# Performance work log

Measured on AMD Instinct MI355X. Metric: run time of the kernel, lower is better.

## Reference

```python
import jax, jax.numpy as jnp
import numpy as np

B, T, D, H = 4, 2048, 1024, 16
HD = D // H  # head_dim = 64


def setup_inputs() -> dict:
    key = jax.random.key(0)
    k1, k2, k3 = jax.random.split(key, 3)
    x = jax.random.normal(k1, (B, T, D), dtype=jnp.float32)
    # torch Linear weights: [out_features, in_features], kaiming-ish scale
    Wqkv = jax.random.normal(k2, (3 * D, D), dtype=jnp.float32) * (1.0 / np.sqrt(D))
    Wout = jax.random.normal(k3, (D, D), dtype=jnp.float32) * (1.0 / np.sqrt(D))
    return {"x": x, "Wqkv": Wqkv, "Wout": Wout}


def reference(x, Wqkv, Wout):
    b, t, c = x.shape
    qkv = x @ Wqkv.T                      # [B,T,3D]
    q, k, v = jnp.split(qkv, 3, axis=2)
    # [B,T,D] -> [B,H,T,HD]
    q = q.reshape(b, t, H, HD).transpose(0, 2, 1, 3)
    k = k.reshape(b, t, H, HD).transpose(0, 2, 1, 3)
    v = v.reshape(b, t, H, HD).transpose(0, 2, 1, 3)
    scale = 1.0 / np.sqrt(HD).astype(np.float32)
    att = jnp.einsum('bhqd,bhkd->bhqk', q, k) * scale  # [B,H,T,T]
    causal = jnp.tril(jnp.ones((t, t), dtype=bool))
    att = jnp.where(causal[None, None], att, -jnp.inf)
    att = jax.nn.softmax(att, axis=-1)
    y = jnp.einsum('bhqk,bhkd->bhqd', att, v)          # [B,H,T,HD]
    y = y.transpose(0, 2, 1, 3).reshape(b, t, c)       # [B,T,D]
    return y @ Wout.T
```

## Files before the change

### kernel.cpp

```cpp
#include <hip/hip_runtime.h>
#include <hip/hip_bf16.h>
#include <stdint.h>

#define B_ 4
#define T_ 2048
#define D_ 1024
#define H_ 16
#define M_ (B_*T_)
#define N1_ (3*D_)

typedef __attribute__((ext_vector_type(8))) short short8;
typedef __attribute__((ext_vector_type(4))) short short4v;
typedef __attribute__((ext_vector_type(4))) float f32x4;
typedef __attribute__((ext_vector_type(16))) float f32x16;

typedef const __attribute__((address_space(1))) void* as1cp;
typedef __attribute__((address_space(3))) void* as3p;

__device__ __forceinline__ ushort f2bf(float f) {
  union { float f; unsigned u; } v; v.f = f;
  unsigned r = v.u + 0x7fffu + ((v.u >> 16) & 1u);
  return (ushort)(r >> 16);
}

__global__ void cast_f32_bf16(const float* __restrict__ in, ushort* __restrict__ out, int n4) {
  int i = blockIdx.x * blockDim.x + threadIdx.x;
  int stride = gridDim.x * blockDim.x;
  for (; i < n4; i += stride) {
    float4 v = reinterpret_cast<const float4*>(in)[i];
    ushort4 o;
    o.x = f2bf(v.x); o.y = f2bf(v.y); o.z = f2bf(v.z); o.w = f2bf(v.w);
    reinterpret_cast<ushort4*>(out)[i] = o;
  }
}

__device__ __forceinline__ void gload_lds16(const ushort* g, ushort* l) {
  __builtin_amdgcn_global_load_lds((as1cp)(const void*)g, (as3p)(void*)l, 16, 0, 0);
}

__device__ __forceinline__ short4v ds_tr16(unsigned addr) {
  short4v r;
  asm volatile("ds_read_b64_tr_b16 %0, %1" : "=v"(r) : "v"(addr) : "memory");
  return r;
}

__device__ __forceinline__ short8 cat8(short4v a, short4v b) {
  short8 r;
  r[0]=a[0]; r[1]=a[1]; r[2]=a[2]; r[3]=a[3];
  r[4]=b[0]; r[5]=b[1]; r[6]=b[2]; r[7]=b[3];
  return r;
}

__device__ __forceinline__ unsigned cvtpk(float lo, float hi) {
  unsigned r;
  asm("v_cvt_pk_bf16_f32 %0, %1, %2" : "=v"(r) : "v"(lo), "v"(hi));
  return r;
}

__device__ __forceinline__ f32x16 mfma32(short8 a, short8 b, f32x16 c) {
  return __builtin_amdgcn_mfma_f32_32x32x16_bf16(a, b, c, 0, 0, 0);
}

template<int MODE>
__global__ __launch_bounds__(256) void gemm_bt(const ushort* __restrict__ A,
                                               const ushort* __restrict__ Bm,
                                               void* __restrict__ Cout,
                                               int M, int N, int K) {
  __shared__ ushort Al[128*32];
  __shared__ ushort Bl[128*32];
  const int tid  = threadIdx.x;
  const int lane = tid & 63;
  const int w    = tid >> 6;
  const int g    = lane >> 4;
  const int ln   = lane & 15;
  const int m0 = blockIdx.y * 128;
  const int n0 = blockIdx.x * 128;
  const int wr = w >> 1, wc = w & 1;

  f32x4 acc[4][4] = {};

  for (int kt = 0; kt < K; kt += 32) {
    __syncthreads();
    #pragma unroll
    for (int j = 0; j < 2; ++j) {
      int cc  = w * 2 + j;
      int idx = cc * 64 + lane;
      int row = idx >> 2;
      int kofs = (idx & 3) * 8;
      gload_lds16(A  + (size_t)(m0 + row) * K + kt + kofs, &Al[cc * 512]);
      gload_lds16(Bm + (size_t)(n0 + row) * K + kt + kofs, &Bl[cc * 512]);
    }
    __syncthreads();
    short8 a[4], b[4];
    #pragma unroll
    for (int m = 0; m < 4; ++m)
      a[m] = *(const short8*)&Al[(wr*64 + m*16 + ln) * 32 + g*8];
    #pragma unroll
    for (int n = 0; n < 4; ++n)
      b[n] = *(const short8*)&Bl[(wc*64 + n*16 + ln) * 32 + g*8];
    #pragma unroll
    for (int m = 0; m < 4; ++m)
      #pragma unroll
      for (int n = 0; n < 4; ++n)
        acc[m][n] = __builtin_amdgcn_mfma_f32_16x16x32_bf16(a[m], b[n], acc[m][n], 0, 0, 0);
  }

  #pragma unroll
  for (int m = 0; m < 4; ++m) {
    int gr = m0 + wr*64 + m*16 + g*4;
    #pragma unroll
    for (int n = 0; n < 4; ++n) {
      int gc = n0 + wc*64 + n*16 + ln;
      #pragma unroll
      for (int r = 0; r < 4; ++r) {
        float v = acc[m][n][r];
        if (MODE == 2 && gc < 1024) v *= 0.18033688011112042f;
        if (MODE) ((ushort*)Cout)[(size_t)(gr + r) * N + gc] = f2bf(v);
        else      ((float*)Cout)[(size_t)(gr + r) * N + gc]  = v;
      }
    }
  }
}

__global__ __launch_bounds__(512, 2) void attn7(const ushort* __restrict__ qkv,
                                                ushort* __restrict__ y) {
  __shared__ ushort Kl[2][4096];
  __shared__ ushort Vl[2][4096];

  const int tid  = threadIdx.x;
  const int lane = tid & 63;
  const int w    = tid >> 6;
  const int l31  = lane & 31;
  const int hi   = lane >> 5;

  const int bh = blockIdx.x;
  const int b  = bh >> 4;
  const int h  = bh & 15;
  const int qb = 7 - (int)blockIdx.y;
  const int rowg = b * T_;
  const int q0 = qb * 256;
  const int qw = q0 + w * 32;
  const int qrow = qw + l31;
  const int nt = 4 * qb + 4;

  const int krow  = tid >> 3;
  const int kslot = tid & 7;
  const int kcb   = (kslot * 16) ^ ((krow & 7) << 4);
  const int vdh = tid & 1, vr = (tid >> 1) & 3, vg = (tid >> 3) & 3,
            vkq = (tid >> 5) & 1, vks = (tid >> 6) & 3, vdt = (tid >> 8) & 1;
  const int vkey = vks*16 + vkq*8 + (vg >> 1)*4 + vr;
  const int vdd  = vdt*32 + (vg & 1)*16 + vdh*8;

  short8 qf[4];
  {
    const ushort* qp = qkv + (size_t)(rowg + qrow) * N1_ + h*64 + hi*8;
    #pragma unroll
    for (int kc = 0; kc < 4; ++kc) qf[kc] = *(const short8*)(qp + kc*16);
  }

  f32x16 oacc[2] = {};
  float lrun = 0.f;

  const unsigned VbBase = (unsigned)(size_t)(as3p)(void*)&Vl[0][0];
  const unsigned trln = (unsigned)(((lane >> 4) * 128) + (lane & 15) * 8);

  gload_lds16(qkv + (size_t)(rowg + 0 + krow) * N1_ + D_ + h*64 + (kcb >> 1), &Kl[0][w*512]);
  gload_lds16(qkv + (size_t)(rowg + 0 + vkey) * N1_ + 2*D_ + h*64 + vdd,      &Vl[0][w*512]);

  for (int kt = 0; kt < nt; ++kt) {
    const int buf = kt & 1;
    const int kbase = kt * 64;
    if (kt + 1 < nt) {
      const int kb2 = kbase + 64;
      gload_lds16(qkv + (size_t)(rowg + kb2 + krow) * N1_ + D_ + h*64 + (kcb >> 1), &Kl[buf^1][w*512]);
      gload_lds16(qkv + (size_t)(rowg + kb2 + vkey) * N1_ + 2*D_ + h*64 + vdd,      &Vl[buf^1][w*512]);
      asm volatile("s_waitcnt vmcnt(2)" ::: "memory");
    } else {
      asm volatile("s_waitcnt vmcnt(0)" ::: "memory");
    }
    asm volatile("s_barrier" ::: "memory");

    const bool act = (kbase <= qw + 31);
    if (act) {
      f32x16 sv[2] = {};
      const char* Kb = (const char*)&Kl[buf][0];
      __builtin_amdgcn_s_setprio(1);
      #pragma unroll
      for (int kc = 0; kc < 4; ++kc) {
        unsigned co = (unsigned)((kc*32 + hi*16) ^ ((l31 & 7) << 4));
        short8 k0 = *(const short8*)(Kb + (size_t)l31*128 + co);
        short8 k1 = *(const short8*)(Kb + (size_t)(32 + l31)*128 + co);
        sv[0] = mfma32(k0, qf[kc], sv[0]);
        sv[1] = mfma32(k1, qf[kc], sv[1]);
      }
      __builtin_amdgcn_s_setprio(0);

      if (kbase + 63 > qw) {
        #pragma unroll
        for (int t = 0; t < 2; ++t)
          #pragma unroll
          for (int r = 0; r < 16; ++r) {
            int kl = kbase + t*32 + (r & 3) + 8*(r >> 2) + 4*hi;
            if (kl > qrow) sv[t][r] = -1.0e38f;
          }
      }

      #pragma unroll
      for (int t = 0; t < 2; ++t)
        #pragma unroll
        for (int r = 0; r < 16; ++r) sv[t][r] = exp2f(sv[t][r] - 12.0f);
      float ts[8];
      #pragma unroll
      for (int r = 0; r < 8; ++r)
        ts[r] = (sv[0][r] + sv[0][r+8]) + (sv[1][r] + sv[1][r+8]);
      lrun += ((ts[0] + ts[1]) + (ts[2] + ts[3])) + ((ts[4] + ts[5]) + (ts[6] + ts[7]));

      const unsigned Vb = VbBase + (unsigned)(buf * 8192);
      short4v vt[2][4][2];
      #pragma unroll
      for (int dt = 0; dt < 2; ++dt)
        #pragma unroll
        for (int ks = 0; ks < 4; ++ks) {
          unsigned a = Vb + (unsigned)(dt*4096 + ks*1024) + trln;
          vt[dt][ks][0] = ds_tr16(a);
          vt[dt][ks][1] = ds_tr16(a + 512);
        }

      short8 pa[4];
      #pragma unroll
      for (int ks = 0; ks < 4; ++ks) {
        const int t = ks >> 1, base = 8 * (ks & 1);
        union { unsigned u[4]; short8 v; } uu;
        uu.u[0] = cvtpk(sv[t][base+0], sv[t][base+1]);
        uu.u[1] = cvtpk(sv[t][base+2], sv[t][base+3]);
        uu.u[2] = cvtpk(sv[t][base+4], sv[t][base+5]);
        uu.u[3] = cvtpk(sv[t][base+6], sv[t][base+7]);
        pa[ks] = uu.v;
      }

      asm volatile("s_waitcnt lgkmcnt(0)" ::: "memory");
      __builtin_amdgcn_sched_barrier(0);
      __builtin_amdgcn_s_setprio(1);
      #pragma unroll
      for (int ks = 0; ks < 4; ++ks) {
        oacc[0] = mfma32(cat8(vt[0][ks][0], vt[0][ks][1]), pa[ks], oacc[0]);
        oacc[1] = mfma32(cat8(vt[1][ks][0], vt[1][ks][1]), pa[ks], oacc[1]);
      }
      __builtin_amdgcn_s_setprio(0);
    }
    asm volatile("s_barrier" ::: "memory");
  }

  float ltot = lrun + __shfl_xor(lrun, 32);
  const float inv = 1.0f / ltot;
  #pragma unroll
  for (int dt = 0; dt < 2; ++dt) {
    #pragma unroll
    for (int rq = 0; rq < 4; ++rq) {
      ushort4 pk4;
      pk4.x = f2bf(oacc[dt][rq*4+0] * inv);
      pk4.y = f2bf(oacc[dt][rq*4+1] * inv);
      pk4.z = f2bf(oacc[dt][rq*4+2] * inv);
      pk4.w = f2bf(oacc[dt][rq*4+3] * inv);
      *(ushort4*)&y[(size_t)(rowg + qrow) * D_ + h*64 + dt*32 + rq*8 + hi*4] = pk4;
    }
  }
}

extern "C" void kernel_launch(void* const* d_in, const int* in_sizes, int n_in,
                              void* d_out, int out_size, void* d_ws, size_t ws_size,
                              hipStream_t stream) {
  const float* x    = (const float*)d_in[0];
  const float* Wqkv = (const float*)d_in[1];
  const float* Wout = (const float*)d_in[2];

  ushort* xb    = (ushort*)d_ws;
  ushort* wqkvb = xb    + (size_t)M_ * D_;
  ushort* woutb = wqkvb + (size_t)N1_ * D_;
  ushort* qkvb  = woutb + (size_t)D_ * D_;
  ushort* yb    = qkvb  + (size_t)M_ * N1_;

  cast_f32_bf16<<<1024, 256, 0, stream>>>(x,    xb,    M_ * D_ / 4);
  cast_f32_bf16<<<512,  256, 0, stream>>>(Wqkv, wqkvb, N1_ * D_ / 4);
  cast_f32_bf16<<<256,  256, 0, stream>>>(Wout, woutb, D_ * D_ / 4);

  gemm_bt<2><<<dim3(N1_/128, M_/128), 256, 0, stream>>>(xb, wqkvb, qkvb, M_, N1_, D_);

  attn7<<<dim3(B_*H_, 8), 512, 0, stream>>>(qkvb, yb);

  gemm_bt<0><<<dim3(D_/128, M_/128), 256, 0, stream>>>(yb, woutb, d_out, M_, D_, D_);
}
```

Measured before the change: 196.6 us.

## Fuse cast kernels, swizzle GEMM tiles across XCDs, reorder attention block scheduling

Merges the three f32-to-bf16 cast launches into one kernel so fewer launches are issued. GEMM grids become 1D, and block IDs are remapped so that consecutive tiles land on the same XCD (id&7 round-robin), which should improve L2 reuse of A and B tiles. Attention blocks are flattened to 1D. Heavy causal query blocks (7..4) are scheduled first, then light ones (0..3), to balance load. The new index arithmetic adds a little cost, and the tile remap assumes the grid size is divisible by 8.

```diff
diff --git a/kernel.cpp b/kernel.cpp
--- a/kernel.cpp
+++ b/kernel.cpp
@@ -23,14 +23,21 @@
   return (ushort)(r >> 16);
 }
 
-__global__ void cast_f32_bf16(const float* __restrict__ in, ushort* __restrict__ out, int n4) {
+__global__ void cast3_f32_bf16(const float* __restrict__ a, ushort* __restrict__ oa, int na,
+                               const float* __restrict__ b, ushort* __restrict__ ob, int nb,
+                               const float* __restrict__ c, ushort* __restrict__ oc, int nc) {
   int i = blockIdx.x * blockDim.x + threadIdx.x;
   int stride = gridDim.x * blockDim.x;
-  for (; i < n4; i += stride) {
-    float4 v = reinterpret_cast<const float4*>(in)[i];
+  int ntot = na + nb + nc;
+  for (; i < ntot; i += stride) {
+    const float* src; ushort* dst; int j = i;
+    if (j < na) { src = a; dst = oa; }
+    else if ((j -= na) < nb) { src = b; dst = ob; }
+    else { j -= nb; src = c; dst = oc; }
+    float4 v = reinterpret_cast<const float4*>(src)[j];
     ushort4 o;
     o.x = f2bf(v.x); o.y = f2bf(v.y); o.z = f2bf(v.z); o.w = f2bf(v.w);
-    reinterpret_cast<ushort4*>(out)[i] = o;
+    reinterpret_cast<ushort4*>(dst)[j] = o;
   }
 }
 
@@ -65,7 +72,7 @@
 __global__ __launch_bounds__(256) void gemm_bt(const ushort* __restrict__ A,
                                                const ushort* __restrict__ Bm,
                                                void* __restrict__ Cout,
-                                               int M, int N, int K) {
+                                               int M, int N, int K, int gx) {
   __shared__ ushort Al[128*32];
   __shared__ ushort Bl[128*32];
   const int tid  = threadIdx.x;
@@ -73,8 +80,13 @@
   const int w    = tid >> 6;
   const int g    = lane >> 4;
   const int ln   = lane & 15;
-  const int m0 = blockIdx.y * 128;
-  const int n0 = blockIdx.x * 128;
+
+  const int nwg = gridDim.x;
+  const int cpx = nwg >> 3;
+  const int id  = (int)blockIdx.x;
+  const int swz = (id & 7) * cpx + (id >> 3);
+  const int m0 = (swz / gx) * 128;
+  const int n0 = (swz % gx) * 128;
   const int wr = w >> 1, wc = w & 1;
 
   f32x4 acc[4][4] = {};
@@ -122,7 +134,7 @@
   }
 }
 
-__global__ __launch_bounds__(512, 2) void attn7(const ushort* __restrict__ qkv,
+__global__ __launch_bounds__(512, 2) void attn8(const ushort* __restrict__ qkv,
                                                 ushort* __restrict__ y) {
   __shared__ ushort Kl[2][4096];
   __shared__ ushort Vl[2][4096];
@@ -133,10 +145,12 @@
   const int l31  = lane & 31;
   const int hi   = lane >> 5;
 
-  const int bh = blockIdx.x;
+  const int L = (int)blockIdx.x;
+  int bh, qb;
+  if (L < 256) { bh = L & 63; qb = 7 - (L >> 6); }
+  else         { int l2 = L - 256; bh = l2 & 63; qb = l2 >> 6; }
   const int b  = bh >> 4;
   const int h  = bh & 15;
-  const int qb = 7 - (int)blockIdx.y;
   const int rowg = b * T_;
   const int q0 = qb * 256;
   const int qw = q0 + w * 32;
@@ -280,13 +294,13 @@
   ushort* qkvb  = woutb + (size_t)D_ * D_;
   ushort* yb    = qkvb  + (size_t)M_ * N1_;
 
-  cast_f32_bf16<<<1024, 256, 0, stream>>>(x,    xb,    M_ * D_ / 4);
-  cast_f32_bf16<<<512,  256, 0, stream>>>(Wqkv, wqkvb, N1_ * D_ / 4);
-  cast_f32_bf16<<<256,  256, 0, stream>>>(Wout, woutb, D_ * D_ / 4);
-
-  gemm_bt<2><<<dim3(N1_/128, M_/128), 256, 0, stream>>>(xb, wqkvb, qkvb, M_, N1_, D_);
-
-  attn7<<<dim3(B_*H_, 8), 512, 0, stream>>>(qkvb, yb);
-
-  gemm_bt<0><<<dim3(D_/128, M_/128), 256, 0, stream>>>(yb, woutb, d_out, M_, D_, D_);
-}
+  cast3_f32_bf16<<<2048, 256, 0, stream>>>(x, xb, M_ * D_ / 4,
+                                           Wqkv, wqkvb, N1_ * D_ / 4,
+                                           Wout, woutb, D_ * D_ / 4);
+
+  gemm_bt<2><<<(N1_/128)*(M_/128), 256, 0, stream>>>(xb, wqkvb, qkvb, M_, N1_, D_, N1_/128);
+
+  attn8<<<512, 512, 0, stream>>>(qkvb, yb);
+
+  gemm_bt<0><<<(D_/128)*(M_/128), 256, 0, stream>>>(yb, woutb, d_out, M_, D_, D_, D_/128);
+}
```

New measurement: 203.6 us. 1.04x slower.
